# Kernel optimization log

Hardware: AMD Instinct MI355X
Metric: run time of the kernel (lower is better)

## Reference

```python
import jax, jax.numpy as jnp
import numpy as np

OFFSET_FP32 = np.uint32(1064828928)  # L-mul exponent-bias correction constant for float32


def lmul_matmul(A, B):
    """Approximate A @ B (m,n)x(n,p) via integer-add-as-multiply on float bit patterns.

    Torch ref adds bit patterns in int64 then truncates with .to(torch.uint32),
    i.e. arithmetic mod 2**32 -- identical to plain uint32 wraparound addition,
    so we stay in uint32 and avoid needing x64 mode.
    """
    Au = jax.lax.bitcast_convert_type(A, jnp.uint32)          # (m, n)
    Bu = jax.lax.bitcast_convert_type(B, jnp.uint32)          # (n, p)
    prod_bits = Au[:, :, None] + Bu[None, :, :] - OFFSET_FP32  # (m, n, p), wraps mod 2^32
    prod = jax.lax.bitcast_convert_type(prod_bits, jnp.float32)
    return prod.sum(axis=1)                                    # (m, p)


def setup_inputs() -> dict:
    key = jax.random.key(0)
    k1, k2, k3 = jax.random.split(key, 3)
    m, n, p = 256, 512, 512
    x = jax.random.normal(k1, (m, n), dtype=jnp.float32)
    bound = 1.0 / np.sqrt(n)  # kaiming_uniform(a=sqrt(5)) -> U(-1/sqrt(fan_in), 1/sqrt(fan_in))
    weight = jax.random.uniform(k2, (p, n), dtype=jnp.float32, minval=-bound, maxval=bound)
    bias = jax.random.uniform(k3, (p,), dtype=jnp.float32, minval=-bound, maxval=bound)
    return {"x": x, "weight": weight, "bias": bias}


def reference(x, weight, bias):
    out = lmul_matmul(x, weight.T)
    return out + bias
```

## Files before the change

kernel.cpp:

```cpp
#include <hip/hip_runtime.h>
#include <stdint.h>


#define OFFSET_FP32 1064828928u

constexpr int M = 256;
constexpr int N = 512;
constexpr int P = 512;

constexpr int BP = 128;
constexpr int BM = 8;
constexpr int TM = 4;
constexpr int KS = 4;
constexpr int KT = N / KS;

__global__ __launch_bounds__(256) void lmul_linear_kernel(
    const uint32_t* __restrict__ xb,
    const uint32_t* __restrict__ wb,
    const float*    __restrict__ bias,
    float*          __restrict__ out)
{
    __shared__ uint32_t Bs[BP * KT];

    const int tid     = threadIdx.x;
    const int p_local = tid & (BP - 1);
    const int m_quad  = __builtin_amdgcn_readfirstlane(tid >> 7);

    const int p0 = blockIdx.y * BP;
    const int m0 = blockIdx.x * BM + m_quad * TM;
    const int k0 = blockIdx.z * KT;

    const int sg = tid & 31;
    const int sr = tid >> 5;
    const uint32_t* wbase = wb + (size_t)p0 * N + k0;
    #pragma unroll
    for (int j = 0; j < 16; ++j) {
        const int pp = sr + j * 8;
        uint4 v = *(const uint4*)(wbase + (size_t)pp * N + sg * 4);
        v.x -= OFFSET_FP32; v.y -= OFFSET_FP32;
        v.z -= OFFSET_FP32; v.w -= OFFSET_FP32;
        const int g = sg ^ (pp & 7);
        *(uint4*)&Bs[pp * KT + g * 4] = v;
    }
    __syncthreads();

    const uint32_t* xr0 = xb + (size_t)(m0 + 0) * N + k0;
    const uint32_t* xr1 = xb + (size_t)(m0 + 1) * N + k0;
    const uint32_t* xr2 = xb + (size_t)(m0 + 2) * N + k0;
    const uint32_t* xr3 = xb + (size_t)(m0 + 3) * N + k0;

    float acc[TM][4] = {};
    const uint32_t* brow = &Bs[p_local * KT];
    const int rot = p_local & 7;

    #pragma unroll 8
    for (int j = 0; j < KT / 4; ++j) {
        const uint4 b  = *(const uint4*)&brow[(j ^ rot) * 4];
        const uint4 a0 = *(const uint4*)(xr0 + j * 4);
        const uint4 a1 = *(const uint4*)(xr1 + j * 4);
        const uint4 a2 = *(const uint4*)(xr2 + j * 4);
        const uint4 a3 = *(const uint4*)(xr3 + j * 4);
        acc[0][0] += __uint_as_float(a0.x + b.x);
        acc[0][1] += __uint_as_float(a0.y + b.y);
        acc[0][2] += __uint_as_float(a0.z + b.z);
        acc[0][3] += __uint_as_float(a0.w + b.w);
        acc[1][0] += __uint_as_float(a1.x + b.x);
        acc[1][1] += __uint_as_float(a1.y + b.y);
        acc[1][2] += __uint_as_float(a1.z + b.z);
        acc[1][3] += __uint_as_float(a1.w + b.w);
        acc[2][0] += __uint_as_float(a2.x + b.x);
        acc[2][1] += __uint_as_float(a2.y + b.y);
        acc[2][2] += __uint_as_float(a2.z + b.z);
        acc[2][3] += __uint_as_float(a2.w + b.w);
        acc[3][0] += __uint_as_float(a3.x + b.x);
        acc[3][1] += __uint_as_float(a3.y + b.y);
        acc[3][2] += __uint_as_float(a3.z + b.z);
        acc[3][3] += __uint_as_float(a3.w + b.w);
    }

    const int p  = p0 + p_local;
    const float bv = (k0 == 0) ? bias[p] : 0.0f;
    #pragma unroll
    for (int r = 0; r < TM; ++r) {
        const float s = (acc[r][0] + acc[r][1]) + (acc[r][2] + acc[r][3]) + bv;
        atomicAdd(&out[(size_t)(m0 + r) * P + p], s);
    }
}

extern "C" void kernel_launch(void* const* d_in, const int* in_sizes, int n_in,
                              void* d_out, int out_size, void* d_ws, size_t ws_size,
                              hipStream_t stream) {
    const uint32_t* xb   = (const uint32_t*)d_in[0];
    const uint32_t* wb   = (const uint32_t*)d_in[1];
    const float*    bias = (const float*)d_in[2];
    float*          out  = (float*)d_out;

    hipMemsetAsync(d_out, 0, (size_t)out_size * sizeof(float), stream);

    dim3 grid(M / BM, P / BP, KS);
    dim3 block(256);
    lmul_linear_kernel<<<grid, block, 0, stream>>>(xb, wb, bias, out);
}
```

Before: 64.38 us.

## Drop split-K atomics and stream weight chunks into LDS via async global_load_lds

Removes the split-K dimension and atomics, and with them the memset launch. Each block now computes full-K outputs for 64 columns and 8 rows and writes them directly. Weight tiles for all four K chunks are staged into LDS with global_load_lds, issuing the next chunk while the current one is computed. The offset subtraction moves from staging to the inner loop on the x operand. This adds ALU work per element and changes the reduction order, and the global_load_lds lane-to-address mapping with swizzle is delicate, so correctness of the LDS layout is a risk.

```diff
diff --git a/kernel.cpp b/kernel.cpp
--- a/kernel.cpp
+++ b/kernel.cpp
@@ -8,11 +8,11 @@
 constexpr int N = 512;
 constexpr int P = 512;
 
-constexpr int BP = 128;
+constexpr int BP = 64;
 constexpr int BM = 8;
-constexpr int TM = 4;
-constexpr int KS = 4;
-constexpr int KT = N / KS;
+constexpr int TM = 2;
+constexpr int KC = 128;
+constexpr int NC = N / KC;
 
 __global__ __launch_bounds__(256) void lmul_linear_kernel(
     const uint32_t* __restrict__ xb,
@@ -20,70 +20,71 @@
     const float*    __restrict__ bias,
     float*          __restrict__ out)
 {
-    __shared__ uint32_t Bs[BP * KT];
+    __shared__ uint32_t Bs[NC][BP][KC];
 
     const int tid     = threadIdx.x;
     const int p_local = tid & (BP - 1);
-    const int m_quad  = __builtin_amdgcn_readfirstlane(tid >> 7);
+    const int wq      = __builtin_amdgcn_readfirstlane(tid >> 6);
 
     const int p0 = blockIdx.y * BP;
-    const int m0 = blockIdx.x * BM + m_quad * TM;
-    const int k0 = blockIdx.z * KT;
+    const int m0 = blockIdx.x * BM + wq * TM;
 
-    const int sg = tid & 31;
-    const int sr = tid >> 5;
-    const uint32_t* wbase = wb + (size_t)p0 * N + k0;
-    #pragma unroll
-    for (int j = 0; j < 16; ++j) {
-        const int pp = sr + j * 8;
-        uint4 v = *(const uint4*)(wbase + (size_t)pp * N + sg * 4);
-        v.x -= OFFSET_FP32; v.y -= OFFSET_FP32;
-        v.z -= OFFSET_FP32; v.w -= OFFSET_FP32;
-        const int g = sg ^ (pp & 7);
-        *(uint4*)&Bs[pp * KT + g * 4] = v;
-    }
+    const int lane  = tid & 63;
+    const int gran  = lane & 31;
+    const int rhalf = lane >> 5;
+
+    auto stage = [&](int c) {
+        #pragma unroll
+        for (int i = 0; i < 8; ++i) {
+            const int row = wq * 16 + i * 2 + rhalf;
+            const uint32_t* src = wb + (size_t)(p0 + row) * N + c * KC
+                                     + ((gran ^ (row & 7)) * 4);
+            uint32_t* dst = &Bs[c][wq * 16 + i * 2][0];
+            __builtin_amdgcn_global_load_lds(
+                (const __attribute__((address_space(1))) uint32_t*)src,
+                (__attribute__((address_space(3))) uint32_t*)dst,
+                16, 0, 0);
+        }
+    };
+
+    float acc[TM][4] = {};
+    const int rot = p_local & 7;
+
+    stage(0);
     __syncthreads();
 
-    const uint32_t* xr0 = xb + (size_t)(m0 + 0) * N + k0;
-    const uint32_t* xr1 = xb + (size_t)(m0 + 1) * N + k0;
-    const uint32_t* xr2 = xb + (size_t)(m0 + 2) * N + k0;
-    const uint32_t* xr3 = xb + (size_t)(m0 + 3) * N + k0;
+    #pragma unroll
+    for (int c = 0; c < NC; ++c) {
+        if (c + 1 < NC) stage(c + 1);
 
-    float acc[TM][4] = {};
-    const uint32_t* brow = &Bs[p_local * KT];
-    const int rot = p_local & 7;
+        const uint32_t* brow = &Bs[c][p_local][0];
+        const uint32_t* xr0  = xb + (size_t)(m0 + 0) * N + c * KC;
+        const uint32_t* xr1  = xb + (size_t)(m0 + 1) * N + c * KC;
 
-    #pragma unroll 8
-    for (int j = 0; j < KT / 4; ++j) {
-        const uint4 b  = *(const uint4*)&brow[(j ^ rot) * 4];
-        const uint4 a0 = *(const uint4*)(xr0 + j * 4);
-        const uint4 a1 = *(const uint4*)(xr1 + j * 4);
-        const uint4 a2 = *(const uint4*)(xr2 + j * 4);
-        const uint4 a3 = *(const uint4*)(xr3 + j * 4);
-        acc[0][0] += __uint_as_float(a0.x + b.x);
-        acc[0][1] += __uint_as_float(a0.y + b.y);
-        acc[0][2] += __uint_as_float(a0.z + b.z);
-        acc[0][3] += __uint_as_float(a0.w + b.w);
-        acc[1][0] += __uint_as_float(a1.x + b.x);
-        acc[1][1] += __uint_as_float(a1.y + b.y);
-        acc[1][2] += __uint_as_float(a1.z + b.z);
-        acc[1][3] += __uint_as_float(a1.w + b.w);
-        acc[2][0] += __uint_as_float(a2.x + b.x);
-        acc[2][1] += __uint_as_float(a2.y + b.y);
-        acc[2][2] += __uint_as_float(a2.z + b.z);
-        acc[2][3] += __uint_as_float(a2.w + b.w);
-        acc[3][0] += __uint_as_float(a3.x + b.x);
-        acc[3][1] += __uint_as_float(a3.y + b.y);
-        acc[3][2] += __uint_as_float(a3.z + b.z);
-        acc[3][3] += __uint_as_float(a3.w + b.w);
+        #pragma unroll 8
+        for (int j = 0; j < KC / 4; ++j) {
+            const uint4 b  = *(const uint4*)&brow[(j ^ rot) * 4];
+            const uint4 a0 = *(const uint4*)(xr0 + j * 4);
+            const uint4 a1 = *(const uint4*)(xr1 + j * 4);
+            acc[0][0] += __uint_as_float((a0.x - OFFSET_FP32) + b.x);
+            acc[0][1] += __uint_as_float((a0.y - OFFSET_FP32) + b.y);
+            acc[0][2] += __uint_as_float((a0.z - OFFSET_FP32) + b.z);
+            acc[0][3] += __uint_as_float((a0.w - OFFSET_FP32) + b.w);
+            acc[1][0] += __uint_as_float((a1.x - OFFSET_FP32) + b.x);
+            acc[1][1] += __uint_as_float((a1.y - OFFSET_FP32) + b.y);
+            acc[1][2] += __uint_as_float((a1.z - OFFSET_FP32) + b.z);
+            acc[1][3] += __uint_as_float((a1.w - OFFSET_FP32) + b.w);
+        }
+
+        if (c + 1 < NC) __syncthreads();
     }
 
-    const int p  = p0 + p_local;
-    const float bv = (k0 == 0) ? bias[p] : 0.0f;
+    const int   p  = p0 + p_local;
+    const float bv = bias[p];
     #pragma unroll
     for (int r = 0; r < TM; ++r) {
-        const float s = (acc[r][0] + acc[r][1]) + (acc[r][2] + acc[r][3]) + bv;
-        atomicAdd(&out[(size_t)(m0 + r) * P + p], s);
+        out[(size_t)(m0 + r) * P + p] =
+            (acc[r][0] + acc[r][1]) + (acc[r][2] + acc[r][3]) + bv;
     }
 }
 
@@ -95,9 +96,7 @@
     const float*    bias = (const float*)d_in[2];
     float*          out  = (float*)d_out;
 
-    hipMemsetAsync(d_out, 0, (size_t)out_size * sizeof(float), stream);
-
-    dim3 grid(M / BM, P / BP, KS);
+    dim3 grid(M / BM, P / BP);
     dim3 block(256);
     lmul_linear_kernel<<<grid, block, 0, stream>>>(xb, wb, bias, out);
 }
```

Result: slower. 67.85 us (+5.4%).
